# Performance work log

Hardware: AMD Instinct MI355X
Metric: run time of the kernel (lower is better)

The kernel has to match this reference:

```python
import jax, jax.numpy as jnp
import numpy as np

CELL = 512
DENSE = 2048
PRED = 24 * 24  # predict_ahead * 24
FEAT = 24
FORGET_BIAS = 1.0


def setup_inputs() -> dict:
    key = jax.random.key(0)
    ks = jax.random.split(key, 7)
    B, T = 1024, 512
    s = lambda fan_in: 1.0 / np.sqrt(fan_in)
    return {
        "X": jax.random.normal(ks[0], (B, T, FEAT), dtype=jnp.float32),
        "W_lstm": jax.random.normal(ks[1], (FEAT + CELL, 4 * CELL), dtype=jnp.float32) * s(FEAT + CELL),
        "b_lstm": jnp.zeros((4 * CELL,), dtype=jnp.float32),
        "W_dense": jax.random.normal(ks[2], (CELL, DENSE), dtype=jnp.float32) * s(CELL),
        "b_dense": jnp.zeros((DENSE,), dtype=jnp.float32),
        "W_pred": jax.random.normal(ks[3], (DENSE, PRED), dtype=jnp.float32) * s(DENSE),
        "b_pred": jnp.zeros((PRED,), dtype=jnp.float32),
    }


def reference(X, W_lstm, b_lstm, W_dense, b_dense, W_pred, b_pred):
    B = X.shape[0]
    c0 = jnp.zeros((B, CELL), dtype=X.dtype)
    h0 = jnp.zeros((B, CELL), dtype=X.dtype)

    def step(carry, x_t):
        c, h = carry
        z = jnp.concatenate([x_t, h], axis=1) @ W_lstm + b_lstm  # [B, 4*CELL]
        i, j, f, o = jnp.split(z, 4, axis=1)  # TF BasicLSTMCell gate order
        new_c = c * jax.nn.sigmoid(f + FORGET_BIAS) + jax.nn.sigmoid(i) * jnp.tanh(j)
        new_h = jnp.tanh(new_c) * jax.nn.sigmoid(o)
        return (new_c, new_h), None

    xs = jnp.swapaxes(X, 0, 1)  # [T, B, FEAT]
    (c_T, h_T), _ = jax.lax.scan(step, (c0, h0), xs)
    dense = jax.nn.relu(h_T @ W_dense + b_dense)
    preds = dense @ W_pred + b_pred
    return preds
```

## Files before the change

### kernel.cpp

```cpp
#include <hip/hip_runtime.h>
#include <hip/hip_fp16.h>

#define BATCH 1024
#define SEQ 512
#define NFEAT 24
#define NCELL 512
#define ZC 2048
#define KP 544
#define NCH 17
#define KL 576
#define DENSE_N 2048
#define PRED_N 576
#define NWG 256
#define NGRP 16
#define GWG 16
#define PFD 6
#define NBUF 7

typedef unsigned short u16;
typedef unsigned int u32;
typedef unsigned long long u64;
typedef unsigned short u16x8 __attribute__((ext_vector_type(8)));
typedef _Float16 f16x8 __attribute__((ext_vector_type(8)));
typedef float f32x4 __attribute__((ext_vector_type(4)));

__device__ __forceinline__ float sigm(float x) { return 1.f / (1.f + __expf(-x)); }
__device__ __forceinline__ float ftanh(float x) {
    float t = __expf(-2.f * fabsf(x));
    float r = (1.f - t) / (1.f + t);
    return copysignf(r, x);
}
__device__ __forceinline__ u16 f2h(float v) {
    _Float16 h = (_Float16)v;
    return *(u16*)&h;
}
__device__ __forceinline__ void st16(u16* p, u32 v) {
    asm volatile("global_store_short %0, %1, off sc0 sc1" :: "v"(p), "v"(v) : "memory");
}
__device__ __forceinline__ void st64(u16* p, u64 v) {
    asm volatile("global_store_dwordx2 %0, %1, off sc0 sc1" :: "v"(p), "v"(v) : "memory");
}

__device__ __forceinline__ u32 hword16(int row, int k) {
    int g = row >> 6, w = (row >> 4) & 3, r = row & 15;
    int ch = k >> 5, kk = k & 31;
    return (u32)(((g * 4 + w) * NCH + ch) * 512)
         + (u32)(((r | ((kk >> 3) << 4)) << 3) + (kk & 7));
}

__global__ __launch_bounds__(256) void prep_w(const float* __restrict__ W,
                                              u16* __restrict__ Wt) {
    int o = blockIdx.x * 256 + threadIdx.x;
    if (o >= ZC * KP) return;
    int n = o / KP, k = o % KP;
    float v = 0.f;
    if (k < NCELL)              v = W[(size_t)(NFEAT + k) * ZC + n];
    else if (k < NCELL + NFEAT) v = W[(size_t)(k - NCELL) * ZC + n];
    Wt[o] = f2h(v);
}

__global__ __launch_bounds__(256) void prep_h(const float* __restrict__ X,
                                              u16* __restrict__ H0, u16* __restrict__ H1) {
    int o = blockIdx.x * 256 + threadIdx.x;
    if (o >= BATCH * KP) return;
    int row = o / KP, k = o % KP;
    u16 b = 0;
    if (k >= NCELL && k < NCELL + NFEAT)
        b = f2h(X[(size_t)row * (SEQ * NFEAT) + (k - NCELL)]);
    u32 w = hword16(row, k);
    H0[w] = b;
    H1[w] = 0;
}

__global__ __launch_bounds__(512, 1) void lstm_persist(
    u16* __restrict__ H0, u16* __restrict__ H1,
    const u16* __restrict__ Wt,
    const float* __restrict__ bias,
    const float* __restrict__ X,
    float* __restrict__ hf32,
    int* __restrict__ bar)
{
    extern __shared__ u16 Ws[];

    const int tid = (int)threadIdx.x;
    const int bid = (int)blockIdx.x;
    const int g = bid & 15, nb2 = bid >> 4;
    const int r0 = g * 64;
    const int lane = tid & 63, wv = tid >> 6;
    const int fi = wv >> 1, ci = wv & 1;
    u16* __restrict__ Hs = Ws + 128 * KL;
    int* __restrict__ bcnt   = bar + g * 64;
    int* __restrict__ bepoch = bar + g * 64 + 32;

    for (int e = tid; e < 128 * (KP / 8); e += 512) {
        int col = e / (KP / 8), k8 = (e % (KP / 8)) * 8;
        int n = col >> 4, cl = col & 15;
        int zc = (n & 3) * NCELL + nb2 * 32 + (n >> 2) * 16 + cl;
        int so = k8 ^ ((col & 7) << 3);
        *(u16x8*)&Ws[col * KL + so] = *(const u16x8*)&Wt[(size_t)zc * KP + k8];
    }
    __syncthreads();

    const int cell = nb2 * 32 + ci * 16 + (lane & 15);
    const float bi = bias[cell], bj = bias[NCELL + cell];
    const float bf_ = bias[2 * NCELL + cell], bo = bias[3 * NCELL + cell];

    const int akof = (lane >> 4) * 8;
    const u32 abase = (u32)((g * 4 + fi) * NCH) * 128u + (u32)lane * 2u;

    const u32 esto = (u32)((g * 4 + fi) * NCH + nb2) * 512u + (u32)ci * 256u + (u32)lane * 4u;
    const int hsw = (wv << 8);

#define WSOFF(cb, off) ((cb) * KL + (((off)) ^ (((cb) & 7) << 3)))

    float ct[4] = {};

    for (int t = 0; t < SEQ; ++t) {
        const u64* Hq = (const u64*)((t & 1) ? H1 : H0);
        u16*       Np = (t & 1) ? H0 : H1;

        f32x4 acc[4] = {};
        __attribute__((aligned(16))) u64 fr[NBUF][2];

#define ALOADS(f, ch) do { \
        f[0] = __hip_atomic_load(&Hq[abase + (u32)(ch) * 128u],     __ATOMIC_RELAXED, __HIP_MEMORY_SCOPE_AGENT); \
        f[1] = __hip_atomic_load(&Hq[abase + (u32)(ch) * 128u + 1], __ATOMIC_RELAXED, __HIP_MEMORY_SCOPE_AGENT); \
        } while (0)
#define CCOMP(f, ch) do { \
        f16x8 a = *(const f16x8*)&f[0]; \
        _Pragma("unroll") \
        for (int gt = 0; gt < 4; ++gt) { \
            f16x8 bn = *(const f16x8*)&Ws[WSOFF((ci * 4 + gt) * 16 + (lane & 15), (ch) * 32 + akof)]; \
            acc[gt] = __builtin_amdgcn_mfma_f32_16x16x32_f16(a, bn, acc[gt], 0, 0, 0); \
        } } while (0)

        ALOADS(fr[0], 0); ALOADS(fr[1], 1); ALOADS(fr[2], 2);
        ALOADS(fr[3], 3); ALOADS(fr[4], 4); ALOADS(fr[5], 5);
        #pragma unroll
        for (int ch = 0; ch < NCH; ++ch) {
            if (ch + PFD < NCH) ALOADS(fr[(ch + PFD) % NBUF], ch + PFD);
            CCOMP(fr[ch % NBUF], ch);
        }
#undef ALOADS
#undef CCOMP

        #pragma unroll
        for (int r = 0; r < 4; ++r) {
            int row16 = (lane >> 4) * 4 + r;
            float zi = acc[0][r] + bi;
            float zj = acc[1][r] + bj;
            float zf = acc[2][r] + bf_;
            float zo = acc[3][r] + bo;
            float cn = ct[r] * sigm(zf + 1.0f) + sigm(zi) * ftanh(zj);
            ct[r] = cn;
            float h = ftanh(cn) * sigm(zo);
            Hs[hsw + ((row16 | (((lane >> 3) & 1) << 4)) << 3) + (lane & 7)] = f2h(h);
            if (t == SEQ - 1) {
                int row = r0 + fi * 16 + row16;
                hf32[(size_t)row * NCELL + cell] = h;
            }
        }
        {
            u64 v = *(const u64*)&Hs[hsw + lane * 4];
            st64(&Np[esto], v);
        }
        if (t + 1 < SEQ && tid < 96) {
            int e = nb2 * 96 + tid;
            int rowg = e / 24, kk = e % 24;
            int row = r0 + rowg;
            float v = X[(size_t)row * (SEQ * NFEAT) + (t + 1) * NFEAT + kk];
            int w2 = rowg >> 4, r16 = rowg & 15;
            u32 idx = (u32)((g * 4 + w2) * NCH + 16) * 512u
                    + (u32)(((r16 | ((kk >> 3) << 4)) << 3) + (kk & 7));
            st16(&Np[idx], (u32)f2h(v));
        }

        __syncthreads();
        if (tid == 0) {
            int n = __hip_atomic_fetch_add(bcnt, 1, __ATOMIC_RELAXED, __HIP_MEMORY_SCOPE_AGENT);
            if (n == GWG - 1) {
                __hip_atomic_store(bcnt, 0, __ATOMIC_RELAXED, __HIP_MEMORY_SCOPE_AGENT);
                __hip_atomic_store(bepoch, t + 1, __ATOMIC_RELAXED, __HIP_MEMORY_SCOPE_AGENT);
            } else {
                int spins = 0;
                while (__hip_atomic_load(bepoch, __ATOMIC_RELAXED, __HIP_MEMORY_SCOPE_AGENT) <= t) {
                    __builtin_amdgcn_s_sleep(2);
                    if (++spins > 20000000) break;
                }
            }
        }
        __syncthreads();
    }
}

template <int ACT>
__global__ __launch_bounds__(256) void gemm64(
    const float* __restrict__ A, const float* __restrict__ Wm,
    const float* __restrict__ bias, float* __restrict__ out,
    int M, int N, int K)
{
    __shared__ float Asf[32][65];
    __shared__ float Bsf[32][65];
    const int c0 = blockIdx.x * 64;
    const int r0 = blockIdx.y * 64;
    const int tid = (int)threadIdx.x;
    const int tx = tid & 15, ty = tid >> 4;

    float acc[4][4];
    #pragma unroll
    for (int r = 0; r < 4; ++r) { acc[r][0]=0.f; acc[r][1]=0.f; acc[r][2]=0.f; acc[r][3]=0.f; }

    for (int k0 = 0; k0 < K; k0 += 32) {
        #pragma unroll
        for (int i = 0; i < 8; ++i) {
            int e = tid + 256 * i;
            int row = e >> 5, kk = e & 31;
            Asf[kk][row] = A[(size_t)(r0 + row) * K + k0 + kk];
        }
        #pragma unroll
        for (int i = 0; i < 8; ++i) {
            int e = tid + 256 * i;
            int kk = e >> 6, cl = e & 63;
            Bsf[kk][cl] = Wm[(size_t)(k0 + kk) * N + c0 + cl];
        }
        __syncthreads();
        #pragma unroll
        for (int kk = 0; kk < 32; ++kk) {
            float b0 = Bsf[kk][tx*4], b1 = Bsf[kk][tx*4+1], b2 = Bsf[kk][tx*4+2], b3 = Bsf[kk][tx*4+3];
            #pragma unroll
            for (int r = 0; r < 4; ++r) {
                float a = Asf[kk][ty*4 + r];
                acc[r][0] = fmaf(a, b0, acc[r][0]);
                acc[r][1] = fmaf(a, b1, acc[r][1]);
                acc[r][2] = fmaf(a, b2, acc[r][2]);
                acc[r][3] = fmaf(a, b3, acc[r][3]);
            }
        }
        __syncthreads();
    }
    #pragma unroll
    for (int r = 0; r < 4; ++r) {
        int gr = r0 + ty * 4 + r;
        #pragma unroll
        for (int j = 0; j < 4; ++j) {
            int gc = c0 + tx * 4 + j;
            float v = acc[r][j] + bias[gc];
            if (ACT) v = fmaxf(v, 0.f);
            out[(size_t)gr * N + gc] = v;
        }
    }
}

extern "C" void kernel_launch(void* const* d_in, const int* in_sizes, int n_in,
                              void* d_out, int out_size, void* d_ws, size_t ws_size,
                              hipStream_t stream)
{
    const float* X  = (const float*)d_in[0];
    const float* Wl = (const float*)d_in[1];
    const float* bl = (const float*)d_in[2];
    const float* Wd = (const float*)d_in[3];
    const float* bd = (const float*)d_in[4];
    const float* Wp = (const float*)d_in[5];
    const float* bp = (const float*)d_in[6];
    float* out = (float*)d_out;

    char* p = (char*)d_ws;
    int* bar      = (int*)p; p += 4096;
    float* hf32   = (float*)p; p += (size_t)BATCH * NCELL * 4;
    float* dense  = (float*)p; p += (size_t)BATCH * DENSE_N * 4;
    u16* Wt   = (u16*)p; p += (size_t)ZC * KP * 2;
    u16* H0   = (u16*)p; p += (size_t)BATCH * KP * 2;
    u16* H1   = (u16*)p; p += (size_t)BATCH * KP * 2;

    (void)hipMemsetAsync(bar, 0, 4096, stream);
    prep_w<<<(ZC * KP) / 256, 256, 0, stream>>>(Wl, Wt);
    prep_h<<<(BATCH * KP) / 256, 256, 0, stream>>>(X, H0, H1);

    const int lds_bytes = 128 * KL * 2 + 8 * 256 * 2;
    (void)hipFuncSetAttribute((const void*)lstm_persist,
                              hipFuncAttributeMaxDynamicSharedMemorySize, lds_bytes);
    lstm_persist<<<NWG, 512, lds_bytes, stream>>>(H0, H1, Wt, bl, X, hf32, bar);

    dim3 blk(256);
    gemm64<1><<<dim3(DENSE_N / 64, BATCH / 64), blk, 0, stream>>>(hf32, Wd, bd, dense, BATCH, DENSE_N, NCELL);
    gemm64<0><<<dim3(PRED_N / 64, BATCH / 64), blk, 0, stream>>>(dense, Wp, bp, out, BATCH, PRED_N, DENSE_N);
}
```

Measured before the change: 2.704 ms.

## Split LSTM recurrent K dimension across wave pairs with LDS partial-sum exchange

Each pair of waves previously split the 8 gate column tiles in half and each wave read all 17 K-chunks of the hidden state from global memory. Now each wave computes all 8 column tiles over roughly half the K chunks, so each wave does half the global H loads. The partial sums are then exchanged through an LDS buffer with three extra block barriers. The weight LDS layout also drops the XOR swizzle in favour of a padded row stride of 552. This trades global load latency on the recurrent critical path for extra LDS traffic, more accumulators and more barriers per step, and may reintroduce bank conflicts.

```diff
diff --git a/kernel.cpp b/kernel.cpp
--- a/kernel.cpp
+++ b/kernel.cpp
@@ -8,14 +8,12 @@
 #define ZC 2048
 #define KP 544
 #define NCH 17
-#define KL 576
+#define KL 552
 #define DENSE_N 2048
 #define PRED_N 576
 #define NWG 256
 #define NGRP 16
 #define GWG 16
-#define PFD 6
-#define NBUF 7
 
 typedef unsigned short u16;
 typedef unsigned int u32;
@@ -88,7 +86,8 @@
     const int r0 = g * 64;
     const int lane = tid & 63, wv = tid >> 6;
     const int fi = wv >> 1, ci = wv & 1;
-    u16* __restrict__ Hs = Ws + 128 * KL;
+    float* __restrict__ Exf = (float*)(Ws + 128 * KL);
+    u16*   __restrict__ Hs  = Ws + 128 * KL + 8192;
     int* __restrict__ bcnt   = bar + g * 64;
     int* __restrict__ bepoch = bar + g * 64 + 32;
 
@@ -96,8 +95,7 @@
         int col = e / (KP / 8), k8 = (e % (KP / 8)) * 8;
         int n = col >> 4, cl = col & 15;
         int zc = (n & 3) * NCELL + nb2 * 32 + (n >> 2) * 16 + cl;
-        int so = k8 ^ ((col & 7) << 3);
-        *(u16x8*)&Ws[col * KL + so] = *(const u16x8*)&Wt[(size_t)zc * KP + k8];
+        *(u16x8*)&Ws[col * KL + k8] = *(const u16x8*)&Wt[(size_t)zc * KP + k8];
     }
     __syncthreads();
 
@@ -110,8 +108,7 @@
 
     const u32 esto = (u32)((g * 4 + fi) * NCH + nb2) * 512u + (u32)ci * 256u + (u32)lane * 4u;
     const int hsw = (wv << 8);
-
-#define WSOFF(cb, off) ((cb) * KL + (((off)) ^ (((cb) & 7) << 3)))
+    const int exo = fi * 1024;
 
     float ct[4] = {};
 
@@ -119,8 +116,8 @@
         const u64* Hq = (const u64*)((t & 1) ? H1 : H0);
         u16*       Np = (t & 1) ? H0 : H1;
 
-        f32x4 acc[4] = {};
-        __attribute__((aligned(16))) u64 fr[NBUF][2];
+        f32x4 acc[8] = {};
+        __attribute__((aligned(16))) u64 fr[9][2];
 
 #define ALOADS(f, ch) do { \
         f[0] = __hip_atomic_load(&Hq[abase + (u32)(ch) * 128u],     __ATOMIC_RELAXED, __HIP_MEMORY_SCOPE_AGENT); \
@@ -129,37 +126,70 @@
 #define CCOMP(f, ch) do { \
         f16x8 a = *(const f16x8*)&f[0]; \
         _Pragma("unroll") \
-        for (int gt = 0; gt < 4; ++gt) { \
-            f16x8 bn = *(const f16x8*)&Ws[WSOFF((ci * 4 + gt) * 16 + (lane & 15), (ch) * 32 + akof)]; \
-            acc[gt] = __builtin_amdgcn_mfma_f32_16x16x32_f16(a, bn, acc[gt], 0, 0, 0); \
+        for (int n = 0; n < 8; ++n) { \
+            f16x8 bn = *(const f16x8*)&Ws[(n * 16 + (lane & 15)) * KL + (ch) * 32 + akof]; \
+            acc[n] = __builtin_amdgcn_mfma_f32_16x16x32_f16(a, bn, acc[n], 0, 0, 0); \
         } } while (0)
 
-        ALOADS(fr[0], 0); ALOADS(fr[1], 1); ALOADS(fr[2], 2);
-        ALOADS(fr[3], 3); ALOADS(fr[4], 4); ALOADS(fr[5], 5);
-        #pragma unroll
-        for (int ch = 0; ch < NCH; ++ch) {
-            if (ch + PFD < NCH) ALOADS(fr[(ch + PFD) % NBUF], ch + PFD);
-            CCOMP(fr[ch % NBUF], ch);
+        if (ci == 0) {
+            #pragma unroll
+            for (int i = 0; i < 9; ++i) ALOADS(fr[i], i);
+            #pragma unroll
+            for (int i = 0; i < 9; ++i) CCOMP(fr[i], i);
+        } else {
+            #pragma unroll
+            for (int i = 0; i < 8; ++i) ALOADS(fr[i], i + 9);
+            #pragma unroll
+            for (int i = 0; i < 8; ++i) CCOMP(fr[i], i + 9);
         }
 #undef ALOADS
 #undef CCOMP
 
-        #pragma unroll
-        for (int r = 0; r < 4; ++r) {
-            int row16 = (lane >> 4) * 4 + r;
-            float zi = acc[0][r] + bi;
-            float zj = acc[1][r] + bj;
-            float zf = acc[2][r] + bf_;
-            float zo = acc[3][r] + bo;
-            float cn = ct[r] * sigm(zf + 1.0f) + sigm(zi) * ftanh(zj);
-            ct[r] = cn;
-            float h = ftanh(cn) * sigm(zo);
-            Hs[hsw + ((row16 | (((lane >> 3) & 1) << 4)) << 3) + (lane & 7)] = f2h(h);
-            if (t == SEQ - 1) {
-                int row = r0 + fi * 16 + row16;
-                hf32[(size_t)row * NCELL + cell] = h;
-            }
-        }
+        if (ci == 1) {
+            #pragma unroll
+            for (int n = 0; n < 4; ++n)
+                *(f32x4*)&Exf[exo + (n * 64 + lane) * 4] = acc[n];
+        }
+        __syncthreads();
+        if (ci == 0) {
+            #pragma unroll
+            for (int n = 0; n < 4; ++n)
+                acc[n] += *(const f32x4*)&Exf[exo + (n * 64 + lane) * 4];
+        }
+        __syncthreads();
+        if (ci == 0) {
+            #pragma unroll
+            for (int n = 0; n < 4; ++n)
+                *(f32x4*)&Exf[exo + (n * 64 + lane) * 4] = acc[n + 4];
+        }
+        __syncthreads();
+        if (ci == 1) {
+            #pragma unroll
+            for (int n = 0; n < 4; ++n)
+                acc[n + 4] += *(const f32x4*)&Exf[exo + (n * 64 + lane) * 4];
+        }
+
+#define EPI(A0, A1, A2, A3) do { \
+        _Pragma("unroll") \
+        for (int r = 0; r < 4; ++r) { \
+            int row16 = (lane >> 4) * 4 + r; \
+            float zi = (A0)[r] + bi; \
+            float zj = (A1)[r] + bj; \
+            float zf = (A2)[r] + bf_; \
+            float zo = (A3)[r] + bo; \
+            float cn = ct[r] * sigm(zf + 1.0f) + sigm(zi) * ftanh(zj); \
+            ct[r] = cn; \
+            float h = ftanh(cn) * sigm(zo); \
+            Hs[hsw + ((row16 | (((lane >> 3) & 1) << 4)) << 3) + (lane & 7)] = f2h(h); \
+            if (t == SEQ - 1) { \
+                int row = r0 + fi * 16 + row16; \
+                hf32[(size_t)row * NCELL + cell] = h; \
+            } \
+        } } while (0)
+        if (ci == 0) EPI(acc[0], acc[1], acc[2], acc[3]);
+        else         EPI(acc[4], acc[5], acc[6], acc[7]);
+#undef EPI
+
         {
             u64 v = *(const u64*)&Hs[hsw + lane * 4];
             st64(&Np[esto], v);
@@ -276,7 +306,7 @@
     prep_w<<<(ZC * KP) / 256, 256, 0, stream>>>(Wl, Wt);
     prep_h<<<(BATCH * KP) / 256, 256, 0, stream>>>(X, H0, H1);
 
-    const int lds_bytes = 128 * KL * 2 + 8 * 256 * 2;
+    const int lds_bytes = 128 * KL * 2 + 16384 + 4096;
     (void)hipFuncSetAttribute((const void*)lstm_persist,
                               hipFuncAttributeMaxDynamicSharedMemorySize, lds_bytes);
     lstm_persist<<<NWG, 512, lds_bytes, stream>>>(H0, H1, Wt, bl, X, hf32, bar);
```

New measurement: 3.134 ms. 15.9% more time.
